# Performance work log

Measured on AMD Instinct MI355X. Metric: run time of the kernel, lower is better.

The kernel has to match this reference:

```python
import jax, jax.numpy as jnp
import numpy as np

N_ENT = 1000000
N_REL = 500
DIM = 128
BATCH = 16384


def setup_inputs() -> dict:
    key = jax.random.key(0)
    k1, k2, k3, k4, k5 = jax.random.split(key, 5)
    # sample[:,0]=head entity, [:,1]=relation, [:,2]=tail entity
    heads = jax.random.randint(k1, (BATCH, 1), 0, N_ENT)
    rels = jax.random.randint(k2, (BATCH, 1), 0, N_REL)
    tails = jax.random.randint(k3, (BATCH, 1), 0, N_ENT)
    sample = jnp.concatenate([heads, rels, tails], axis=1).astype(jnp.int64)
    # Xavier-uniform init: bound = sqrt(6/(fan_in+fan_out))
    b_e = float(np.sqrt(6.0 / (N_ENT + DIM)))
    b_r = float(np.sqrt(6.0 / (N_REL + DIM * DIM)))
    entity_embedding = jax.random.uniform(k4, (N_ENT, DIM), jnp.float32, -b_e, b_e)
    relation_embedding = jax.random.uniform(k5, (N_REL, DIM * DIM), jnp.float32, -b_r, b_r)
    return {"sample": sample, "entity_embedding": entity_embedding,
            "relation_embedding": relation_embedding}


def _l2norm(x, axis):
    # matches F.normalize(p=2): x / max(||x||, eps)
    n = jnp.sqrt(jnp.sum(x * x, axis=axis, keepdims=True))
    return x / jnp.maximum(n, 1e-12)


def reference(sample, entity_embedding, relation_embedding):
    h, r, t = sample[:, 0], sample[:, 1], sample[:, 2]
    A = _l2norm(entity_embedding[h], axis=-1)                 # [B, d]
    R = relation_embedding[r].reshape(-1, DIM, DIM)           # [B, d, d]
    A_T = _l2norm(entity_embedding[t], axis=-1)               # [B, d]
    tr = jnp.einsum('bij,bj->bi', R, A_T)                     # [B, d]
    return -jnp.sum(A * tr, axis=-1)                          # [B]
```

## Files before the change

kernel.cpp:

```cpp
#include <hip/hip_runtime.h>

#define DIM   128
#define BATCH 16384
#define NREL  500
#define CHUNK 16
#define SPLIT 4


__global__ void zero_k(int* __restrict__ hist) {
    int i = blockIdx.x * 256 + threadIdx.x;
    if (i < NREL) hist[i] = 0;
}

__global__ void hist_k(const int* __restrict__ sample, int* __restrict__ hist) {
    int i = blockIdx.x * 256 + threadIdx.x;
    if (i < BATCH) atomicAdd(&hist[sample[i * 3 + 1]], 1);
}

__global__ void scan_k(const int* __restrict__ hist, int* __restrict__ off,
                       int* __restrict__ cur) {
    __shared__ int s[512];
    int t = threadIdx.x;
    int orig = (t < NREL) ? hist[t] : 0;
    s[t] = orig;
    __syncthreads();
    #pragma unroll
    for (int d = 1; d < 512; d <<= 1) {
        int x = (t >= d) ? s[t - d] : 0;
        __syncthreads();
        s[t] += x;
        __syncthreads();
    }
    if (t <= NREL) {
        int e = s[t] - orig;
        off[t] = e;
        if (t < NREL) cur[t] = e;
    }
}

__global__ void scat_k(const int* __restrict__ sample, int* __restrict__ cur,
                       int* __restrict__ ids) {
    int i = blockIdx.x * 256 + threadIdx.x;
    if (i < BATCH) {
        int r = sample[i * 3 + 1];
        int p = atomicAdd(&cur[r], 1);
        ids[p] = i;
    }
}

__global__ __launch_bounds__(256, 3)
void score_k(const int* __restrict__ sample, const float* __restrict__ ent,
             const float* __restrict__ rel, const int* __restrict__ off,
             const int* __restrict__ ids, float* __restrict__ out) {
    const int blk = blockIdx.x;
    const int g   = blk >> 2;
    const int sub = blk & 3;
    const int s0 = off[g], s1 = off[g + 1];
    const int m  = s1 - s0;
    if (m == 0) return;
    const int chunk = (m + SPLIT - 1) >> 2;
    const int lo = s0 + sub * chunk;
    const int hi = min(s1, lo + chunk);
    if (lo >= hi) return;
    const int cnt = hi - lo;

    const int tid  = threadIdx.x;
    const int lane = tid & 63;
    const int wave = tid >> 6;
    const int row  = tid >> 1;
    const int half = tid & 1;

    const float4* __restrict__ R4 = (const float4*)(rel + (size_t)g * (DIM * DIM));
    float4 Rr[16];
    #pragma unroll
    for (int q = 0; q < 16; ++q)
        Rr[q] = R4[row * 32 + half * 16 + q];

    __shared__ alignas(16) float sAT[CHUNK * 2 * DIM];
    __shared__ float sInv[CHUNK * 2];
    __shared__ float sRed[CHUNK * 4];
    __shared__ int   sIds[CHUNK];

    for (int base = 0; base < cnt; base += CHUNK) {
        const int cact = min(CHUNK, cnt - base);

        #pragma unroll
        for (int p = 0; p < 4; ++p) {
            int c = p * 4 + wave;
            if (c < cact) {
                int gi = ids[lo + base + c];
                if (lane == 0) sIds[c] = gi;
                int eidx = (lane < 32) ? sample[gi * 3 + 0] : sample[gi * 3 + 2];
                int e    = (lane & 31) * 4;
                float4 v = *(const float4*)(ent + (size_t)eidx * DIM + e);
                *(float4*)&sAT[c * 256 + (lane < 32 ? 0 : DIM) + e] = v;
                float sq = v.x * v.x + v.y * v.y + v.z * v.z + v.w * v.w;
                #pragma unroll
                for (int o = 16; o > 0; o >>= 1) sq += __shfl_xor(sq, o);
                if ((lane & 31) == 0)
                    sInv[c * 2 + (lane >> 5)] = 1.0f / fmaxf(sqrtf(sq), 1e-12f);
            }
        }
        __syncthreads();

        for (int c0 = 0; c0 < cact; c0 += 2) {
            const int c1 = (c0 + 1 < cact) ? c0 + 1 : c0;
            const float4* Ta = (const float4*)&sAT[c0 * 256 + DIM + half * 64];
            const float4* Tb = (const float4*)&sAT[c1 * 256 + DIM + half * 64];
            float a0 = 0.f, a1 = 0.f;
            #pragma unroll
            for (int q = 0; q < 16; ++q) {
                float4 ta = Ta[q], tb = Tb[q];
                a0 = fmaf(Rr[q].x, ta.x, a0); a1 = fmaf(Rr[q].x, tb.x, a1);
                a0 = fmaf(Rr[q].y, ta.y, a0); a1 = fmaf(Rr[q].y, tb.y, a1);
                a0 = fmaf(Rr[q].z, ta.z, a0); a1 = fmaf(Rr[q].z, tb.z, a1);
                a0 = fmaf(Rr[q].w, ta.w, a0); a1 = fmaf(Rr[q].w, tb.w, a1);
            }
            float p0 = sAT[c0 * 256 + row] * a0;
            float p1 = sAT[c1 * 256 + row] * a1;
            #pragma unroll
            for (int o = 32; o > 0; o >>= 1) {
                p0 += __shfl_down(p0, o);
                p1 += __shfl_down(p1, o);
            }
            if (lane == 0) {
                sRed[c0 * 4 + wave] = p0;
                if (c1 != c0) sRed[c1 * 4 + wave] = p1;
            }
        }
        __syncthreads();

        if (tid < cact) {
            float s = sRed[tid * 4] + sRed[tid * 4 + 1]
                    + sRed[tid * 4 + 2] + sRed[tid * 4 + 3];
            out[sIds[tid]] = -s * sInv[tid * 2] * sInv[tid * 2 + 1];
        }
        __syncthreads();
    }
}

extern "C" void kernel_launch(void* const* d_in, const int* in_sizes, int n_in,
                              void* d_out, int out_size, void* d_ws, size_t ws_size,
                              hipStream_t stream) {
    const int*   sample = (const int*)d_in[0];
    const float* ent    = (const float*)d_in[1];
    const float* rel    = (const float*)d_in[2];
    float*       out    = (float*)d_out;
    int*         ws     = (int*)d_ws;

    int* hist = ws;
    int* off  = ws + 512;
    int* cur  = ws + 1536;
    int* ids  = ws + 2048;

    zero_k<<<2, 256, 0, stream>>>(hist);
    hist_k<<<BATCH / 256, 256, 0, stream>>>(sample, hist);
    scan_k<<<1, 512, 0, stream>>>(hist, off, cur);
    scat_k<<<BATCH / 256, 256, 0, stream>>>(sample, cur, ids);
    score_k<<<NREL * SPLIT, 256, 0, stream>>>(sample, ent, rel, off, ids, out);
}
```

Baseline: 613.8 us.

## Fuse bucketing kernels into one single-block prep kernel and prefetch entity ids

Replaces the four preprocessing launches (zero, histogram, scan, scatter) with a single 1024-thread block that builds the histogram, scan and scatter in shared memory, cutting launch count and global atomics. The score kernel now maps block index to relation as blk % NREL so the split sub-blocks of one relation are spread across the grid instead of adjacent. It also stages sample ids and entity indices into shared memory before the gather, removing the dependent global loads per wave at the cost of extra barriers. The single-block prep serializes the 16K-element pass on one CU.

```diff
diff --git a/kernel.cpp b/kernel.cpp
--- a/kernel.cpp
+++ b/kernel.cpp
@@ -7,43 +7,36 @@
 #define SPLIT 4
 
 
-__global__ void zero_k(int* __restrict__ hist) {
-    int i = blockIdx.x * 256 + threadIdx.x;
-    if (i < NREL) hist[i] = 0;
-}
-
-__global__ void hist_k(const int* __restrict__ sample, int* __restrict__ hist) {
-    int i = blockIdx.x * 256 + threadIdx.x;
-    if (i < BATCH) atomicAdd(&hist[sample[i * 3 + 1]], 1);
-}
-
-__global__ void scan_k(const int* __restrict__ hist, int* __restrict__ off,
-                       int* __restrict__ cur) {
-    __shared__ int s[512];
-    int t = threadIdx.x;
-    int orig = (t < NREL) ? hist[t] : 0;
-    s[t] = orig;
+__global__ __launch_bounds__(1024)
+void prep_k(const int* __restrict__ sample, int* __restrict__ off,
+            int* __restrict__ ids) {
+    __shared__ int sh[NREL];
+    __shared__ int sc[512];
+    const int t = threadIdx.x;
+    if (t < NREL) sh[t] = 0;
+    __syncthreads();
+    for (int i = t; i < BATCH; i += 1024)
+        atomicAdd(&sh[sample[i * 3 + 1]], 1);
+    __syncthreads();
+    if (t < 512) sc[t] = (t < NREL) ? sh[t] : 0;
     __syncthreads();
     #pragma unroll
     for (int d = 1; d < 512; d <<= 1) {
-        int x = (t >= d) ? s[t - d] : 0;
+        int x = (t < 512 && t >= d) ? sc[t - d] : 0;
         __syncthreads();
-        s[t] += x;
+        if (t < 512) sc[t] += x;
         __syncthreads();
     }
-    if (t <= NREL) {
-        int e = s[t] - orig;
+    if (t < NREL) {
+        int e = sc[t] - sh[t];
         off[t] = e;
-        if (t < NREL) cur[t] = e;
+        sh[t]  = e;
     }
-}
-
-__global__ void scat_k(const int* __restrict__ sample, int* __restrict__ cur,
-                       int* __restrict__ ids) {
-    int i = blockIdx.x * 256 + threadIdx.x;
-    if (i < BATCH) {
+    if (t == 0) off[NREL] = BATCH;
+    __syncthreads();
+    for (int i = t; i < BATCH; i += 1024) {
         int r = sample[i * 3 + 1];
-        int p = atomicAdd(&cur[r], 1);
+        int p = atomicAdd(&sh[r], 1);
         ids[p] = i;
     }
 }
@@ -53,12 +46,12 @@
              const float* __restrict__ rel, const int* __restrict__ off,
              const int* __restrict__ ids, float* __restrict__ out) {
     const int blk = blockIdx.x;
-    const int g   = blk >> 2;
-    const int sub = blk & 3;
+    const int g   = blk % NREL;
+    const int sub = blk / NREL;
     const int s0 = off[g], s1 = off[g + 1];
     const int m  = s1 - s0;
     if (m == 0) return;
-    const int chunk = (m + SPLIT - 1) >> 2;
+    const int chunk = (m + SPLIT - 1) / SPLIT;
     const int lo = s0 + sub * chunk;
     const int hi = min(s1, lo + chunk);
     if (lo >= hi) return;
@@ -80,17 +73,22 @@
     __shared__ float sInv[CHUNK * 2];
     __shared__ float sRed[CHUNK * 4];
     __shared__ int   sIds[CHUNK];
+    __shared__ int   sEid[CHUNK * 2];
 
     for (int base = 0; base < cnt; base += CHUNK) {
         const int cact = min(CHUNK, cnt - base);
+
+        if (tid < cact) sIds[tid] = ids[lo + base + tid];
+        __syncthreads();
+        if (tid < cact * 2)
+            sEid[tid] = sample[sIds[tid >> 1] * 3 + (tid & 1) * 2];
+        __syncthreads();
 
         #pragma unroll
         for (int p = 0; p < 4; ++p) {
             int c = p * 4 + wave;
             if (c < cact) {
-                int gi = ids[lo + base + c];
-                if (lane == 0) sIds[c] = gi;
-                int eidx = (lane < 32) ? sample[gi * 3 + 0] : sample[gi * 3 + 2];
+                int eidx = sEid[c * 2 + (lane < 32 ? 0 : 1)];
                 int e    = (lane & 31) * 4;
                 float4 v = *(const float4*)(ent + (size_t)eidx * DIM + e);
                 *(float4*)&sAT[c * 256 + (lane < 32 ? 0 : DIM) + e] = v;
@@ -148,14 +146,9 @@
     float*       out    = (float*)d_out;
     int*         ws     = (int*)d_ws;
 
-    int* hist = ws;
-    int* off  = ws + 512;
-    int* cur  = ws + 1536;
-    int* ids  = ws + 2048;
+    int* off = ws;
+    int* ids = ws + 512;
 
-    zero_k<<<2, 256, 0, stream>>>(hist);
-    hist_k<<<BATCH / 256, 256, 0, stream>>>(sample, hist);
-    scan_k<<<1, 512, 0, stream>>>(hist, off, cur);
-    scat_k<<<BATCH / 256, 256, 0, stream>>>(sample, cur, ids);
+    prep_k<<<1, 1024, 0, stream>>>(sample, off, ids);
     score_k<<<NREL * SPLIT, 256, 0, stream>>>(sample, ent, rel, off, ids, out);
 }
```

New measurement: 618.5 us. No clear change (+0.8%).
